# Kernel optimization log

Measured on AMD Instinct MI355X. Metric: run time of the kernel, lower is better.

The kernel has to match this reference:

```python
import jax, jax.numpy as jnp
import numpy as np

DIM = 2048
N_HEADS = 32
N_KV_HEADS = 8
HEAD_DIM = 64
REPEATS = N_HEADS // N_KV_HEADS
SLIDING_WINDOW = 1024
EPS = 1e-6
B, T = 2, 2048


def _alibi_slopes(n):
    # n_heads=32 is a power of 2
    r = 2.0 ** (-8.0 / n)
    return jnp.asarray([r ** i for i in range(n)], dtype=jnp.float32)


def _rms_norm(x, w, eps):
    # RMSNorm over the last (flattened heads*head_dim) axis
    var = jnp.mean(x * x, axis=-1, keepdims=True)
    return x * jax.lax.rsqrt(var + eps) * w


def setup_inputs() -> dict:
    key = jax.random.key(0)
    ks = jax.random.split(key, 6)
    s = 0.02
    return {
        "x": jax.random.normal(ks[0], (B, T, DIM), jnp.float32),
        "wq": jax.random.normal(ks[1], (N_HEADS * HEAD_DIM, DIM), jnp.float32) * s,
        "wk": jax.random.normal(ks[2], (N_KV_HEADS * HEAD_DIM, DIM), jnp.float32) * s,
        "wv": jax.random.normal(ks[3], (N_KV_HEADS * HEAD_DIM, DIM), jnp.float32) * s,
        "wo": jax.random.normal(ks[4], (DIM, N_HEADS * HEAD_DIM), jnp.float32) * s,
        "q_norm_w": jnp.ones((N_HEADS * HEAD_DIM,), jnp.float32),
        "k_norm_w": jnp.ones((N_KV_HEADS * HEAD_DIM,), jnp.float32),
    }


def reference(x, wq, wk, wv, wo, q_norm_w, k_norm_w):
    bsz, seqlen, _ = x.shape
    xq = _rms_norm(x @ wq.T, q_norm_w, EPS)
    xk = _rms_norm(x @ wk.T, k_norm_w, EPS)
    xv = x @ wv.T
    xq = xq.reshape(bsz, seqlen, N_HEADS, HEAD_DIM).transpose(0, 2, 1, 3)  # b h t d
    xk = xk.reshape(bsz, seqlen, N_KV_HEADS, HEAD_DIM).transpose(0, 2, 1, 3)
    xv = xv.reshape(bsz, seqlen, N_KV_HEADS, HEAD_DIM).transpose(0, 2, 1, 3)
    # GQA: repeat_interleave kv heads
    xk = jnp.repeat(xk, REPEATS, axis=1)
    xv = jnp.repeat(xv, REPEATS, axis=1)

    pos = jnp.arange(seqlen)
    dist = pos[None, :] - pos[:, None]                     # [t,s] = s - t (<=0 on causal side)
    slopes = _alibi_slopes(N_HEADS)
    alibi = slopes[:, None, None] * dist.astype(jnp.float32)  # [h,t,s]
    allowed = (dist <= 0) & (dist >= -SLIDING_WINDOW)      # causal + sliding window
    bias = jnp.where(allowed[None], alibi, -jnp.inf)       # [h,t,s]

    scale = 1.0 / jnp.sqrt(jnp.asarray(HEAD_DIM, jnp.float32))
    scores = jnp.einsum("bhtd,bhsd->bhts", xq, xk) * scale + bias[None]
    attn = jax.nn.softmax(scores, axis=-1)
    out = jnp.einsum("bhts,bhsd->bhtd", attn, xv)          # [b,h,t,d]
    out = out.transpose(0, 2, 1, 3).reshape(bsz, seqlen, N_HEADS * HEAD_DIM)
    return out @ wo.T
```

## Files before the change

### kernel.cpp

```cpp
#include <hip/hip_runtime.h>


typedef _Float16 f16;
typedef __attribute__((ext_vector_type(8))) _Float16 f16x8;
typedef __attribute__((ext_vector_type(4))) _Float16 f16x4;
typedef __attribute__((ext_vector_type(2))) _Float16 f16x2;
typedef __attribute__((ext_vector_type(4))) float f32x4;

#define T_ 2048
#define NH 32
#define NKV 8
#define HD 64
#define WINDOW 1024
#define EPS_ 1e-6f
#define LOG2E 1.44269504088896340736f
#define LDQKV 3072

__device__ inline void async16(void* lds, const void* g) {
  __builtin_amdgcn_global_load_lds(
      (const __attribute__((address_space(1))) unsigned int*)g,
      (__attribute__((address_space(3))) unsigned int*)lds, 16, 0, 0);
}

struct CvtArgs {
  const float* src[5];
  f16* dst[5];
  int n4[5];
};
__global__ __launch_bounds__(256) void cvt_multi(CvtArgs a) {
  const int seg = blockIdx.y;
  const float* in = a.src[seg];
  f16* out = a.dst[seg];
  const int n4 = a.n4[seg];
  for (int i = blockIdx.x * blockDim.x + threadIdx.x; i < n4;
       i += gridDim.x * blockDim.x) {
    float4 v = ((const float4*)in)[i];
    f16x4 o;
    o[0] = (f16)v.x; o[1] = (f16)v.y; o[2] = (f16)v.z; o[3] = (f16)v.w;
    ((f16x4*)out)[i] = o;
  }
}


#define DSRD(p, off) (*(const f16x8*)((p) + (off)))

template <int BN>
__global__ __launch_bounds__(512, 2) void gemm_nt8(const f16* __restrict__ A,
                                                   const f16* __restrict__ B,
                                                   void* __restrict__ C,
                                                   int M, int N, int K, int ldc,
                                                   int out_f32) {
  constexpr int WN = BN / 4;
  constexpr int JN = WN / 32;
  constexpr int RB = BN / 64;
  constexpr int BUFB = BN * 128;
  extern __shared__ char smem[];
  f16* sA = (f16*)smem;
  f16* sB = (f16*)(smem + 65536);

  const int gx = gridDim.x;
  const int nwg = gx * gridDim.y;
  int bid = blockIdx.y * gx + blockIdx.x;
  if (!(nwg & 7)) bid = (bid & 7) * (nwg >> 3) + (bid >> 3);
  const int m0 = (bid / gx) * 256;
  const int n0 = (bid % gx) * BN;

  const int tid = threadIdx.x;
  const int lane = tid & 63;
  const int wave = tid >> 6;
  const int quad = lane >> 4, l16 = lane & 15;
  const int wm = wave >> 2, wn = wave & 3;

  const int srow = tid >> 3;
  const int sgr = (((tid & 7) ^ (srow & 7))) * 8;
  const f16* gA = A + (size_t)(m0 + srow) * K + sgr;
  const f16* gB = B + (size_t)(n0 + srow) * K + sgr;
  const size_t r64 = (size_t)64 * K;

  const char* cA = (const char*)sA;
  const char* cB = (const char*)sB;
  const int xm = (l16 & 7) << 4;
  const int xk0 = (quad * 16) ^ xm;
  const int xk1 = (64 + quad * 16) ^ xm;
  const int abase = (wm * 128 + l16) * 128;
  const int bbase = (wn * WN + l16) * 128;

  f32x4 acc[8][2 * JN] = {};
  const int nt = K >> 6;

#pragma unroll
  for (int a = 0; a < 4; ++a)
    async16(sA + a * 4096 + tid * 8, gA + (size_t)a * r64);
#pragma unroll
  for (int rb = 0; rb < RB; ++rb)
    async16(sB + rb * 4096 + tid * 8, gB + (size_t)rb * r64);
  asm volatile("s_waitcnt vmcnt(0)" ::: "memory");
  __builtin_amdgcn_s_barrier();

  for (int t = 0; t < nt; ++t) {
    const int bufoA = (t & 1) << 15;
    const int bufoB = (t & 1) * BUFB;
    f16* sAn = sA + (((t & 1) ^ 1) << 14);
    f16* sBn = sB + ((t & 1) ^ 1) * (BUFB / 2);
    const bool st = (t + 1 < nt);
    const size_t gk = (size_t)(t + 1) * 64;

    f16x8 af[4][2], bf[JN][2];

    auto ldA = [&](int mh) {
#pragma unroll
      for (int i = 0; i < 4; ++i) {
        af[i][0] = DSRD(cA, bufoA + abase + mh * 8192 + i * 2048 + xk0);
        af[i][1] = DSRD(cA, bufoA + abase + mh * 8192 + i * 2048 + xk1);
      }
    };
    auto ldB = [&](int nh) {
#pragma unroll
      for (int j = 0; j < JN; ++j) {
        bf[j][0] = DSRD(cB, bufoB + bbase + nh * (WN / 2) * 128 + j * 2048 + xk0);
        bf[j][1] = DSRD(cB, bufoB + bbase + nh * (WN / 2) * 128 + j * 2048 + xk1);
      }
    };
    auto mm = [&](int mh, int nh) {
      __builtin_amdgcn_s_barrier();
      asm volatile("s_waitcnt lgkmcnt(0)" ::: "memory");
      __builtin_amdgcn_sched_barrier(0);
      __builtin_amdgcn_s_setprio(1);
#pragma unroll
      for (int i = 0; i < 4; ++i) {
#pragma unroll
        for (int j = 0; j < JN; ++j) {
          acc[mh * 4 + i][nh * JN + j] = __builtin_amdgcn_mfma_f32_16x16x32_f16(
              af[i][0], bf[j][0], acc[mh * 4 + i][nh * JN + j], 0, 0, 0);
          acc[mh * 4 + i][nh * JN + j] = __builtin_amdgcn_mfma_f32_16x16x32_f16(
              af[i][1], bf[j][1], acc[mh * 4 + i][nh * JN + j], 0, 0, 0);
        }
      }
      __builtin_amdgcn_s_setprio(0);
    };

    ldA(0); ldB(0);
    if (st) {
      async16(sAn + 0 * 4096 + tid * 8, gA + 0 * r64 + gk);
      async16(sAn + 1 * 4096 + tid * 8, gA + 1 * r64 + gk);
      async16(sBn + 0 * 4096 + tid * 8, gB + 0 * r64 + gk);
      if (RB == 4) async16(sBn + 1 * 4096 + tid * 8, gB + 1 * r64 + gk);
    }
    mm(0, 0);
    __builtin_amdgcn_s_barrier();

    ldB(1);
    if (st) {
      async16(sAn + 2 * 4096 + tid * 8, gA + 2 * r64 + gk);
      async16(sAn + 3 * 4096 + tid * 8, gA + 3 * r64 + gk);
      if (RB == 4) {
        async16(sBn + 2 * 4096 + tid * 8, gB + 2 * r64 + gk);
        async16(sBn + 3 * 4096 + tid * 8, gB + 3 * r64 + gk);
      } else {
        async16(sBn + 1 * 4096 + tid * 8, gB + 1 * r64 + gk);
      }
    }
    mm(0, 1);
    __builtin_amdgcn_s_barrier();

    ldA(1); ldB(0);
    mm(1, 0);
    __builtin_amdgcn_s_barrier();

    ldB(1);
    mm(1, 1);
    if (st) asm volatile("s_waitcnt vmcnt(0)" ::: "memory");
    __builtin_amdgcn_s_barrier();
  }

#pragma unroll
  for (int im = 0; im < 8; ++im) {
    const int row0 = m0 + wm * 128 + im * 16 + quad * 4;
#pragma unroll
    for (int jn = 0; jn < 2 * JN; ++jn) {
      const int col = n0 + wn * WN + jn * 16 + l16;
#pragma unroll
      for (int r = 0; r < 4; ++r) {
        const float v = acc[im][jn][r];
        if (out_f32) ((float*)C)[(size_t)(row0 + r) * ldc + col] = v;
        else         ((f16*)C)[(size_t)(row0 + r) * ldc + col] = (f16)v;
      }
    }
  }
}

__global__ __launch_bounds__(256) void rmsnorm2(f16* __restrict__ xqkv,
                                                const float* __restrict__ qw,
                                                const float* __restrict__ kw) {
  __shared__ float red[4];
  const int which = blockIdx.y;
  const int tid = threadIdx.x;

  auto block_sum = [&](float ss) -> float {
#pragma unroll
    for (int off = 32; off > 0; off >>= 1) ss += __shfl_down(ss, off);
    if ((tid & 63) == 0) red[tid >> 6] = ss;
    __syncthreads();
    return red[0] + red[1] + red[2] + red[3];
  };

  if (which == 0) {
    f16* p = xqkv + (size_t)blockIdx.x * LDQKV;
    f16x8 v = ((const f16x8*)p)[tid];
    float f[8];
    float ss = 0.f;
#pragma unroll
    for (int j = 0; j < 8; ++j) { f[j] = (float)v[j]; ss += f[j] * f[j]; }
    const float scale = rsqrtf(block_sum(ss) / 2048.0f + EPS_);
    const float4 w0 = ((const float4*)qw)[tid * 2];
    const float4 w1 = ((const float4*)qw)[tid * 2 + 1];
    f16x8 o;
    o[0] = (f16)(f[0] * scale * w0.x); o[1] = (f16)(f[1] * scale * w0.y);
    o[2] = (f16)(f[2] * scale * w0.z); o[3] = (f16)(f[3] * scale * w0.w);
    o[4] = (f16)(f[4] * scale * w1.x); o[5] = (f16)(f[5] * scale * w1.y);
    o[6] = (f16)(f[6] * scale * w1.z); o[7] = (f16)(f[7] * scale * w1.w);
    ((f16x8*)p)[tid] = o;
  } else {
    f16* p = xqkv + (size_t)blockIdx.x * LDQKV + 2048;
    f16x2 v = ((const f16x2*)p)[tid];
    const float f0 = (float)v[0], f1 = (float)v[1];
    const float scale = rsqrtf(block_sum(f0 * f0 + f1 * f1) / 512.0f + EPS_);
    const float2 w = ((const float2*)kw)[tid];
    f16x2 o;
    o[0] = (f16)(f0 * scale * w.x);
    o[1] = (f16)(f1 * scale * w.y);
    ((f16x2*)p)[tid] = o;
  }
}

__global__ __launch_bounds__(256) void kvfrag(const f16* __restrict__ xqkv,
                                              f16* __restrict__ Kf,
                                              f16* __restrict__ Vf) {
  __shared__ f16 Lk[64][72];
  __shared__ f16 Lv[64][72];
  const int kt = blockIdx.x;
  const int b = blockIdx.y >> 3, kh = blockIdx.y & 7;
  const int t0 = kt * 64;
  const int tid = threadIdx.x;
  const int r = tid >> 3, c = (tid & 7) * 8;
#pragma unroll
  for (int rp = 0; rp < 2; ++rp) {
    const int rr = r + rp * 32;
    const f16* src = xqkv + (size_t)(b * T_ + t0 + rr) * LDQKV + kh * 64 + c;
    *(f16x8*)(&Lk[rr][c]) = *(const f16x8*)(src + 2048);
    *(f16x8*)(&Lv[rr][c]) = *(const f16x8*)(src + 2560);
  }
  __syncthreads();
  const size_t obase = ((size_t)(b * 8 + kh) * 32 + kt) * 4096;
#pragma unroll
  for (int cc0 = 0; cc0 < 2; ++cc0) {
    const int cc = tid + cc0 * 256;
    const int nb = cc >> 7, kc = (cc >> 6) & 1, ln = cc & 63;
    const int qd = ln >> 4, s16 = ln & 15;
    *(f16x8*)(Kf + obase + cc * 8) = *(const f16x8*)(&Lk[nb * 16 + s16][kc * 32 + qd * 8]);
    f16x8 o;
#pragma unroll
    for (int j = 0; j < 8; ++j) o[j] = Lv[kc * 32 + qd * 8 + j][nb * 16 + s16];
    *(f16x8*)(Vf + obase + cc * 8) = o;
  }
}

__global__ __launch_bounds__(256, 8) void attn(const f16* __restrict__ Q,
                                               const f16* __restrict__ Kf,
                                               const f16* __restrict__ Vf,
                                               f16* __restrict__ O) {
  constexpr int LDW = 72;
  __shared__ f16 Qs[64 * LDW];
  __shared__ float Lx[4][16];

  const int qt = blockIdx.x, h = blockIdx.y, b = blockIdx.z;
  const int kh = h >> 2;
  const int q0 = qt * 64;
  const int tid = threadIdx.x;
  const int lane = tid & 63, wave = tid >> 6;
  const int quad = lane >> 4, l16 = lane & 15;
  const float scale2 = 0.125f * LOG2E;
  const float slope2 = exp2f(-0.25f * (float)h) * LOG2E;
  const float M2 = 10.0f;

  const int sr = tid >> 3, sc = (tid & 7) * 8;

#pragma unroll
  for (int rp = 0; rp < 2; ++rp) {
    const int rr = sr + rp * 32;
    *(f16x8*)(Qs + rr * LDW + sc) =
        *(const f16x8*)(Q + (size_t)(b * T_ + q0 + rr) * LDQKV + h * HD + sc);
  }
  __syncthreads();
  f16x8 qf[2];
#pragma unroll
  for (int kc = 0; kc < 2; ++kc)
    qf[kc] = *(const f16x8*)(Qs + (wave * 16 + l16) * LDW + kc * 32 + quad * 8);
  f16* Ps = Qs + wave * 16 * LDW;

  f32x4 o_acc[4] = {};
  float lsum = 0.f;

  const int kt_lo = (q0 >= WINDOW) ? ((q0 - WINDOW) >> 6) : 0;
  const int my_q = q0 + wave * 16 + l16;
  const f16* kfb = Kf + (size_t)(b * 8 + kh) * 131072 + lane * 8;
  const f16* vfb = Vf + (size_t)(b * 8 + kh) * 131072 + lane * 8;

  float sr4[4];
#pragma unroll
  for (int r = 0; r < 4; ++r) sr4[r] = slope2 * (float)r;
  float base = slope2 * (float)(kt_lo * 64 + quad * 4 - my_q) - M2;
  const float bstep = slope2 * 64.0f;
  const float b16 = slope2 * 16.0f;

  for (int kt = kt_lo; kt <= qt; ++kt) {
    const int k0 = kt * 64;
    const f16* kp = kfb + kt * 4096;
    const f16* vp = vfb + kt * 4096;
    const bool maskt = (kt == qt) || (q0 + 63 - k0 > WINDOW);

    float bnb = base;
#pragma unroll
    for (int nb = 0; nb < 4; ++nb) {
      f32x4 a = {0.f, 0.f, 0.f, 0.f};
#pragma unroll
      for (int kc = 0; kc < 2; ++kc) {
        const f16x8 kfr = *(const f16x8*)(kp + (nb * 2 + kc) * 512);
        a = __builtin_amdgcn_mfma_f32_16x16x32_f16(kfr, qf[kc], a, 0, 0, 0);
      }
      f16x4 pk;
#pragma unroll
      for (int r = 0; r < 4; ++r) {
        float v = fmaf(a[r], scale2, bnb + sr4[r]);
        if (maskt) {
          const int dist = k0 + nb * 16 + quad * 4 + r - my_q;
          if (dist > 0 || dist < -WINDOW) v = -1e30f;
        }
        const float p = __builtin_amdgcn_exp2f(v);
        lsum += p;
        pk[r] = (f16)p;
      }
      *(f16x4*)(Ps + l16 * LDW + nb * 16 + quad * 4) = pk;
      bnb += b16;
    }
    base += bstep;

#pragma unroll
    for (int nb = 0; nb < 4; ++nb) {
#pragma unroll
      for (int kc = 0; kc < 2; ++kc) {
        const f16x8 pa = *(const f16x8*)(Ps + l16 * LDW + kc * 32 + quad * 8);
        const f16x8 vb = *(const f16x8*)(vp + (nb * 2 + kc) * 512);
        o_acc[nb] = __builtin_amdgcn_mfma_f32_16x16x32_f16(pa, vb, o_acc[nb], 0, 0, 0);
      }
    }
  }

  lsum += __shfl_xor(lsum, 16);
  lsum += __shfl_xor(lsum, 32);
  if (quad == 0) Lx[wave][l16] = lsum;
  float rl[4];
#pragma unroll
  for (int r = 0; r < 4; ++r) rl[r] = 1.0f / Lx[wave][quad * 4 + r];

#pragma unroll
  for (int r = 0; r < 4; ++r) {
    const int q = q0 + wave * 16 + quad * 4 + r;
#pragma unroll
    for (int nb = 0; nb < 4; ++nb)
      O[(size_t)(b * T_ + q) * (NH * HD) + h * HD + nb * 16 + l16] =
          (f16)(o_acc[nb][r] * rl[r]);
  }
}

extern "C" void kernel_launch(void* const* d_in, const int* in_sizes, int n_in,
                              void* d_out, int out_size, void* d_ws, size_t ws_size,
                              hipStream_t stream) {
  const float* x  = (const float*)d_in[0];
  const float* wq = (const float*)d_in[1];
  const float* wk = (const float*)d_in[2];
  const float* wv = (const float*)d_in[3];
  const float* wo = (const float*)d_in[4];
  const float* qw = (const float*)d_in[5];
  const float* kw = (const float*)d_in[6];
  float* out = (float*)d_out;

  char* ws = (char*)d_ws;
  size_t off = 0;
  auto carve = [&](size_t bytes) -> char* {
    char* p = ws + off;
    off += (bytes + 255) & ~(size_t)255;
    return p;
  };
  f16* xh    = (f16*)carve((size_t)4096 * 2048 * 2);
  f16* wqkvh = (f16*)carve((size_t)3072 * 2048 * 2);
  f16* woh   = (f16*)carve((size_t)2048 * 2048 * 2);
  f16* xqkv  = (f16*)carve((size_t)4096 * 3072 * 2);
  f16* Kf = wqkvh;
  f16* Vf = wqkvh + (size_t)16 * 131072;
  f16* ao = xh;

  static bool attr_done = false;
  if (!attr_done) {
    (void)hipFuncSetAttribute((const void*)gemm_nt8<256>,
                              hipFuncAttributeMaxDynamicSharedMemorySize,
                              131072);
    (void)hipFuncSetAttribute((const void*)gemm_nt8<128>,
                              hipFuncAttributeMaxDynamicSharedMemorySize,
                              98304);
    attr_done = true;
  }

  CvtArgs ca;
  ca.src[0] = x;  ca.dst[0] = xh;                            ca.n4[0] = (4096 * 2048) / 4;
  ca.src[1] = wq; ca.dst[1] = wqkvh;                         ca.n4[1] = (2048 * 2048) / 4;
  ca.src[2] = wk; ca.dst[2] = wqkvh + (size_t)2048 * 2048;   ca.n4[2] = (512 * 2048) / 4;
  ca.src[3] = wv; ca.dst[3] = wqkvh + (size_t)2560 * 2048;   ca.n4[3] = (512 * 2048) / 4;
  ca.src[4] = wo; ca.dst[4] = woh;                           ca.n4[4] = (2048 * 2048) / 4;
  cvt_multi<<<dim3(1024, 5), 256, 0, stream>>>(ca);

  gemm_nt8<256><<<dim3(12, 16), 512, 131072, stream>>>(xh, wqkvh, xqkv, 4096, 3072, 2048, LDQKV, 0);
  rmsnorm2<<<dim3(4096, 2), 256, 0, stream>>>(xqkv, qw, kw);
  kvfrag<<<dim3(32, 16), 256, 0, stream>>>(xqkv, Kf, Vf);
  attn<<<dim3(32, 32, 2), 256, 0, stream>>>(xqkv, Kf, Vf, ao);
  gemm_nt8<128><<<dim3(16, 16), 512, 98304, stream>>>(ao, woh, out, 4096, 2048, 2048, 2048, 1);
}
```

Baseline: 315.7 us.

## Use 256x192 tiles for QKV GEMM, hoist prefetches, reverse attention tile order

Adds a dedicated QKV projection GEMM with 256x192 tiles, so the grid becomes 16x16 = 256 workgroups instead of 12x16 = 192 and covers more CUs on the 256-CU part. In the generic GEMM, all next-tile async loads are now issued together in the first phase rather than split across two phases. The attention kernel launches query tiles in reverse order, so the longest (late-position) tiles start first and load balance improves. The cost is a larger tile per workgroup at one workgroup per CU, more live registers, and earlier LDS pressure from the hoisted prefetches.

```diff
diff --git a/kernel.cpp b/kernel.cpp
--- a/kernel.cpp
+++ b/kernel.cpp
@@ -41,8 +41,129 @@
   }
 }
 
-
 #define DSRD(p, off) (*(const f16x8*)((p) + (off)))
+
+__global__ __launch_bounds__(512, 1) void gemm_nt192(const f16* __restrict__ A,
+                                                     const f16* __restrict__ B,
+                                                     f16* __restrict__ C) {
+  constexpr int K = 2048, ldc = 3072;
+  extern __shared__ char smem[];
+  f16* sA = (f16*)smem;
+  f16* sB = (f16*)(smem + 65536);
+
+  const int gx = gridDim.x;
+  const int nwg = gx * gridDim.y;
+  int bid = blockIdx.y * gx + blockIdx.x;
+  bid = (bid & 7) * (nwg >> 3) + (bid >> 3);
+  const int m0 = (bid / gx) * 256;
+  const int n0 = (bid % gx) * 192;
+
+  const int tid = threadIdx.x;
+  const int lane = tid & 63;
+  const int wave = tid >> 6;
+  const int quad = lane >> 4, l16 = lane & 15;
+  const int wm = wave >> 2, wn = wave & 3;
+
+  const int srow = tid >> 3;
+  const int sgr = (((tid & 7) ^ (srow & 7))) * 8;
+  const f16* gA = A + (size_t)(m0 + srow) * K + sgr;
+  const f16* gB = B + (size_t)(n0 + srow) * K + sgr;
+  const size_t r64 = (size_t)64 * K;
+
+  const char* cA = (const char*)sA;
+  const char* cB = (const char*)sB;
+  const int xm = (l16 & 7) << 4;
+  const int xk0 = (quad * 16) ^ xm;
+  const int xk1 = (64 + quad * 16) ^ xm;
+  const int abase = (wm * 128 + l16) * 128;
+  const int bbase = (wn * 48 + l16) * 128;
+
+  f32x4 acc[8][3] = {};
+  const int nt = K >> 6;
+
+#pragma unroll
+  for (int a = 0; a < 4; ++a)
+    async16(sA + a * 4096 + tid * 8, gA + (size_t)a * r64);
+#pragma unroll
+  for (int rb = 0; rb < 3; ++rb)
+    async16(sB + rb * 4096 + tid * 8, gB + (size_t)rb * r64);
+  asm volatile("s_waitcnt vmcnt(0)" ::: "memory");
+  __builtin_amdgcn_s_barrier();
+
+  for (int t = 0; t < nt; ++t) {
+    const int bufoA = (t & 1) << 15;
+    const int bufoB = (t & 1) * 24576;
+    f16* sAn = sA + (((t & 1) ^ 1) << 14);
+    f16* sBn = sB + ((t & 1) ^ 1) * 12288;
+    const bool st = (t + 1 < nt);
+    const size_t gk = (size_t)(t + 1) * 64;
+
+    f16x8 af[4], bf[3][2];
+
+    auto ldA = [&](int mh, int xk) {
+#pragma unroll
+      for (int i = 0; i < 4; ++i)
+        af[i] = DSRD(cA, bufoA + abase + mh * 8192 + i * 2048 + xk);
+    };
+    auto mm = [&](int mh, int kc) {
+      __builtin_amdgcn_s_barrier();
+      asm volatile("s_waitcnt lgkmcnt(0)" ::: "memory");
+      __builtin_amdgcn_sched_barrier(0);
+      __builtin_amdgcn_s_setprio(1);
+#pragma unroll
+      for (int i = 0; i < 4; ++i)
+#pragma unroll
+        for (int j = 0; j < 3; ++j)
+          acc[mh * 4 + i][j] = __builtin_amdgcn_mfma_f32_16x16x32_f16(
+              af[i], bf[j][kc], acc[mh * 4 + i][j], 0, 0, 0);
+      __builtin_amdgcn_s_setprio(0);
+    };
+
+    ldA(0, xk0);
+#pragma unroll
+    for (int j = 0; j < 3; ++j) {
+      bf[j][0] = DSRD(cB, bufoB + bbase + j * 2048 + xk0);
+      bf[j][1] = DSRD(cB, bufoB + bbase + j * 2048 + xk1);
+    }
+    if (st) {
+#pragma unroll
+      for (int a = 0; a < 4; ++a)
+        async16(sAn + a * 4096 + tid * 8, gA + a * r64 + gk);
+    }
+    mm(0, 0);
+    __builtin_amdgcn_s_barrier();
+
+    ldA(0, xk1);
+    if (st) {
+#pragma unroll
+      for (int rb = 0; rb < 3; ++rb)
+        async16(sBn + rb * 4096 + tid * 8, gB + rb * r64 + gk);
+    }
+    mm(0, 1);
+    __builtin_amdgcn_s_barrier();
+
+    ldA(1, xk0);
+    mm(1, 0);
+    __builtin_amdgcn_s_barrier();
+
+    ldA(1, xk1);
+    mm(1, 1);
+    if (st) asm volatile("s_waitcnt vmcnt(0)" ::: "memory");
+    __builtin_amdgcn_s_barrier();
+  }
+
+#pragma unroll
+  for (int im = 0; im < 8; ++im) {
+    const int row0 = m0 + wm * 128 + im * 16 + quad * 4;
+#pragma unroll
+    for (int j = 0; j < 3; ++j) {
+      const int col = n0 + wn * 48 + j * 16 + l16;
+#pragma unroll
+      for (int r = 0; r < 4; ++r)
+        C[(size_t)(row0 + r) * ldc + col] = (f16)acc[im][j][r];
+    }
+  }
+}
 
 template <int BN>
 __global__ __launch_bounds__(512, 2) void gemm_nt8(const f16* __restrict__ A,
@@ -141,25 +262,17 @@
 
     ldA(0); ldB(0);
     if (st) {
-      async16(sAn + 0 * 4096 + tid * 8, gA + 0 * r64 + gk);
-      async16(sAn + 1 * 4096 + tid * 8, gA + 1 * r64 + gk);
-      async16(sBn + 0 * 4096 + tid * 8, gB + 0 * r64 + gk);
-      if (RB == 4) async16(sBn + 1 * 4096 + tid * 8, gB + 1 * r64 + gk);
+#pragma unroll
+      for (int a = 0; a < 4; ++a)
+        async16(sAn + a * 4096 + tid * 8, gA + a * r64 + gk);
+#pragma unroll
+      for (int rb = 0; rb < RB; ++rb)
+        async16(sBn + rb * 4096 + tid * 8, gB + rb * r64 + gk);
     }
     mm(0, 0);
     __builtin_amdgcn_s_barrier();
 
     ldB(1);
-    if (st) {
-      async16(sAn + 2 * 4096 + tid * 8, gA + 2 * r64 + gk);
-      async16(sAn + 3 * 4096 + tid * 8, gA + 3 * r64 + gk);
-      if (RB == 4) {
-        async16(sBn + 2 * 4096 + tid * 8, gB + 2 * r64 + gk);
-        async16(sBn + 3 * 4096 + tid * 8, gB + 3 * r64 + gk);
-      } else {
-        async16(sBn + 1 * 4096 + tid * 8, gB + 1 * r64 + gk);
-      }
-    }
     mm(0, 1);
     __builtin_amdgcn_s_barrier();
 
@@ -273,7 +386,8 @@
   __shared__ f16 Qs[64 * LDW];
   __shared__ float Lx[4][16];
 
-  const int qt = blockIdx.x, h = blockIdx.y, b = blockIdx.z;
+  const int qt = 31 - blockIdx.x;
+  const int h = blockIdx.y, b = blockIdx.z;
   const int kh = h >> 2;
   const int q0 = qt * 64;
   const int tid = threadIdx.x;
@@ -402,9 +516,9 @@
 
   static bool attr_done = false;
   if (!attr_done) {
-    (void)hipFuncSetAttribute((const void*)gemm_nt8<256>,
+    (void)hipFuncSetAttribute((const void*)gemm_nt192,
                               hipFuncAttributeMaxDynamicSharedMemorySize,
-                              131072);
+                              114688);
     (void)hipFuncSetAttribute((const void*)gemm_nt8<128>,
                               hipFuncAttributeMaxDynamicSharedMemorySize,
                               98304);
@@ -419,7 +533,7 @@
   ca.src[4] = wo; ca.dst[4] = woh;                           ca.n4[4] = (2048 * 2048) / 4;
   cvt_multi<<<dim3(1024, 5), 256, 0, stream>>>(ca);
 
-  gemm_nt8<256><<<dim3(12, 16), 512, 131072, stream>>>(xh, wqkvh, xqkv, 4096, 3072, 2048, LDQKV, 0);
+  gemm_nt192<<<dim3(16, 16), 512, 114688, stream>>>(xh, wqkvh, xqkv);
   rmsnorm2<<<dim3(4096, 2), 256, 0, stream>>>(xqkv, qw, kw);
   kvfrag<<<dim3(32, 16), 256, 0, stream>>>(xqkv, Kf, Vf);
   attn<<<dim3(32, 32, 2), 256, 0, stream>>>(xqkv, Kf, Vf, ao);
```

Measured after the change: 305.7 us. 3.2% less time.
